# Optimization experiments

Measured on AMD Instinct MI355X. Metric: run time of the kernel, lower is better.

Reference implementation:

```python
import jax, jax.numpy as jnp
import numpy as np
from jax import lax


def setup_inputs() -> dict:
    key = jax.random.key(0)
    ks = jax.random.split(key, 9)
    B, L, d_model = 1, 2048, 1024
    d_inner, d_state, d_conv = 2048, 16, 4

    def g(k, shape, scale):
        return jax.random.normal(k, shape, dtype=jnp.float32) * scale

    return dict(
        x=g(ks[0], (B, L, d_model), 1.0),
        in_proj_w=g(ks[1], (2 * d_inner, d_model), 0.02),   # torch Linear layout (out, in)
        conv_w=g(ks[2], (d_inner, 1, d_conv), 0.1),          # depthwise conv kernel
        conv_b=g(ks[3], (d_inner,), 0.02),
        x_proj_w=g(ks[4], (2 * d_state, d_inner), 0.02),
        dt_proj_w=g(ks[5], (d_inner, d_inner), 0.02),
        dt_proj_b=g(ks[6], (d_inner,), 0.02),
        out_proj_w=g(ks[7], (d_model, d_inner), 0.02),
        A_log=jnp.log(jnp.arange(1, d_state + 1, dtype=jnp.float32)),
        D_param=jnp.ones((d_inner,), dtype=jnp.float32),
    )


def reference(x, in_proj_w, conv_w, conv_b, x_proj_w, dt_proj_w, dt_proj_b,
              out_proj_w, A_log, D_param):
    # x: (B, L, d_model)
    B, L, _ = x.shape
    d_inner = D_param.shape[0]
    d_conv = conv_w.shape[-1]

    xz = x @ in_proj_w.T                       # (B, L, 2*d_inner)
    x_p, z = jnp.split(xz, 2, axis=-1)         # each (B, L, d_inner)

    # causal depthwise conv1d: torch pads d_conv-1 both sides then slices [:L],
    # which equals left-pad d_conv-1 with a valid conv.
    xc = jnp.transpose(x_p, (0, 2, 1))         # (B, d_inner, L)
    xc = lax.conv_general_dilated(
        xc, conv_w, window_strides=(1,), padding=[(d_conv - 1, 0)],
        dimension_numbers=('NCH', 'OIH', 'NCH'), feature_group_count=d_inner)
    xc = xc + conv_b[None, :, None]
    xc = jax.nn.silu(jnp.transpose(xc, (0, 2, 1)))  # (B, L, d_inner)

    # ---- ssm(), mode='tustin'. Note: A_discrete in the original is dead code
    # in tustin mode (never used downstream), so it is omitted.
    dt = jax.nn.softplus(xc @ dt_proj_w.T + dt_proj_b)   # (B, L, d_inner)
    BC = xc @ x_proj_w.T                                 # (B, L, 2*d_state)
    B_ssm, C_ssm = jnp.split(BC, 2, axis=-1)             # (B, L, d_state) each

    # Original: B_disc = dt[...,None] * B_ssm[:, :, None, :]  (B,L,D,N)
    #           y = einsum('bld,bldn->bln', xc, B_disc)
    # This contraction factorizes: sum_d xc*dt is independent of n.
    s = jnp.sum(xc * dt, axis=-1, keepdims=True)          # (B, L, 1)
    y = s * B_ssm                                         # (B, L, d_state)
    y = y * C_ssm                                         # einsum('bln,n->bln', ., ones) * C
    # Original does y.sum(-1) + xc * D; keepdims makes the broadcast well-defined.
    y = jnp.sum(y, axis=-1, keepdims=True) + xc * D_param  # (B, L, d_inner)

    y = y * jax.nn.silu(z)
    return y @ out_proj_w.T                                # (B, L, d_model)
```

## Files before the change

### kernel.cpp

```cpp
#include <hip/hip_runtime.h>
#include <hip/hip_bf16.h>

typedef __attribute__((ext_vector_type(8))) short bf16x8;
typedef __attribute__((ext_vector_type(4))) float f32x4;

__device__ __forceinline__ float b2f(unsigned short u) {
  union { float f; unsigned int i; } v; v.i = ((unsigned int)u) << 16; return v.f;
}
__device__ __forceinline__ unsigned short f2b(float f) {
  __hip_bfloat16 h = __float2bfloat16(f);
  union { __hip_bfloat16 h; unsigned short u; } v; v.h = h; return v.u;
}

#define F32_MAGIC 0x3F800000u

#define GLDS16(g, l)                                                        \
  __builtin_amdgcn_global_load_lds(                                         \
      (const __attribute__((address_space(1))) void*)(g),                   \
      (__attribute__((address_space(3))) void*)(l), 16, 0, 0)

#define POST_BARRIER_FENCE()                  \
  do {                                        \
    asm volatile("" ::: "memory");            \
    __builtin_amdgcn_sched_barrier(0);        \
  } while (0)

__global__ __launch_bounds__(256) void cast4_k(const void* __restrict__ s0, unsigned short* __restrict__ d0,
                                               const void* __restrict__ s1, unsigned short* __restrict__ d1,
                                               const void* __restrict__ s2, unsigned short* __restrict__ d2,
                                               const void* __restrict__ s3, unsigned short* __restrict__ d3,
                                               const unsigned int* __restrict__ dpw) {
  const int i = blockIdx.x * 256 + threadIdx.x;
  const void* s; unsigned short* d; int off;
  if      (i <  262144) { s = s0; d = d0; off = i; }
  else if (i <  786432) { s = s1; d = d1; off = i - 262144; }
  else if (i < 1310720) { s = s2; d = d2; off = i - 786432; }
  else if (i < 1572864) { s = s3; d = d3; off = i - 1310720; }
  else return;
  const bool src_f32 = (dpw[0] == F32_MAGIC);
  bf16x8 o;
  if (src_f32) {
    const float* p = (const float*)s + (size_t)off * 8;
#pragma unroll
    for (int j = 0; j < 8; ++j) o[j] = (short)f2b(p[j]);
  } else {
    o = *(const bf16x8*)((const unsigned short*)s + (size_t)off * 8);
  }
  *(bf16x8*)(d + (size_t)off * 8) = o;
}

__global__ __launch_bounds__(256) void cast_small_k(const void* __restrict__ s0, unsigned short* __restrict__ d0,
                                                    const void* __restrict__ s1, unsigned short* __restrict__ d1,
                                                    const void* __restrict__ s2, unsigned short* __restrict__ d2,
                                                    const void* __restrict__ s3, unsigned short* __restrict__ d3,
                                                    const void* __restrict__ s4, unsigned short* __restrict__ d4,
                                                    const unsigned int* __restrict__ dpw) {
  const int i = blockIdx.x * 256 + threadIdx.x;
  const void* s; unsigned short* d; int off;
  if      (i < 8192) { s = s0; d = d0; off = i; }
  else if (i < 9216) { s = s1; d = d1; off = i - 8192; }
  else if (i < 9472) { s = s2; d = d2; off = i - 9216; }
  else if (i < 9728) { s = s3; d = d3; off = i - 9472; }
  else if (i < 9984) { s = s4; d = d4; off = i - 9728; }
  else return;
  const bool src_f32 = (dpw[0] == F32_MAGIC);
  bf16x8 o;
  if (src_f32) {
    const float* p = (const float*)s + (size_t)off * 8;
#pragma unroll
    for (int j = 0; j < 8; ++j) o[j] = (short)f2b(p[j]);
  } else {
    o = *(const bf16x8*)((const unsigned short*)s + (size_t)off * 8);
  }
  *(bf16x8*)(d + (size_t)off * 8) = o;
}

template <int BM, int BN, int BK, int DEPTH, int MODE, int SWZ>
__global__ __launch_bounds__(256) void gemm_nt(const unsigned short* __restrict__ A,
                                               const unsigned short* __restrict__ B,
                                               void* __restrict__ C,
                                               int M, int N, int K, int gx,
                                               const unsigned short* __restrict__ bias,
                                               const unsigned int* __restrict__ dpw) {
  constexpr int CPR = BK / 8;
  constexpr int CPRL = (BK == 128) ? 4 : (BK == 64) ? 3 : 2;
  constexpr int LPS_A = BM * BK / 2048;
  constexpr int LPS_B = BN * BK / 2048;
  constexpr int LPS = LPS_A + LPS_B;
  constexpr int ASTEP = BM * BK * 2;
  constexpr int BSTEP = BN * BK * 2;
  constexpr int WM = BM / 2, WN = BN / 2;
  constexpr int MI = WM / 16, NJ = WN / 16;
  constexpr int KK = BK / 32;

  __shared__ char lds[DEPTH * (ASTEP + BSTEP)];
  constexpr int BBASE = DEPTH * ASTEP;

  int bx, by;
  if (SWZ) {
    const int bid = blockIdx.x;
    const int k8 = bid & 7;
    const int s = bid >> 3;
    const int sq = k8 + 8 * (s >> 6);
    const int sqw = gx >> 3;
    bx = (sq % sqw) * 8 + (s & 7);
    by = (sq / sqw) * 8 + ((s >> 3) & 7);
  } else {
    bx = blockIdx.x;
    by = blockIdx.y;
  }

  const int tid = threadIdx.x;
  const int lane = tid & 63;
  const int wave = tid >> 6;
  const int m0 = bx * BM;
  const int n0 = by * BN;
  const int wm = (wave >> 1) * WM;
  const int wn = (wave & 1) * WN;
  const int lr = lane & 15;
  const int lu = lane >> 4;

  auto swz = [](int u, int row) {
    int s2 = u ^ (row & (CPR - 1));
    if (CPR == 4) s2 ^= (row >> 2) & 3;
    return s2 & (CPR - 1);
  };

  f32x4 acc[MI][NJ];
#pragma unroll
  for (int i = 0; i < MI; ++i)
#pragma unroll
    for (int j = 0; j < NJ; ++j) acc[i][j] = (f32x4){0.f, 0.f, 0.f, 0.f};

  const unsigned short* aG[LPS_A];
  const unsigned short* bG[LPS_B];
  int aL[LPS_A], bL[LPS_B];
#pragma unroll
  for (int p = 0; p < LPS_A; ++p) {
    const int c = tid + p * 256;
    const int row = c >> CPRL, u = c & (CPR - 1);
    aG[p] = A + (size_t)(m0 + row) * K + swz(u, row) * 8;
    aL[p] = c * 16;
  }
#pragma unroll
  for (int q = 0; q < LPS_B; ++q) {
    const int c = tid + q * 256;
    const int row = c >> CPRL, u = c & (CPR - 1);
    bG[q] = B + (size_t)(n0 + row) * K + swz(u, row) * 8;
    bL[q] = c * 16;
  }
  int aR[MI][KK], bR[NJ][KK];
#pragma unroll
  for (int i = 0; i < MI; ++i)
#pragma unroll
    for (int kk = 0; kk < KK; ++kk) {
      const int row = wm + i * 16 + lr;
      aR[i][kk] = (row * BK + swz(kk * 4 + lu, row) * 8) * 2;
    }
#pragma unroll
  for (int j = 0; j < NJ; ++j)
#pragma unroll
    for (int kk = 0; kk < KK; ++kk) {
      const int row = wn + j * 16 + lr;
      bR[j][kk] = (row * BK + swz(kk * 4 + lu, row) * 8) * 2;
    }

  const int nk = K / BK;

  auto stage = [&](int ab, int bb) {
#pragma unroll
    for (int p = 0; p < LPS_A; ++p) {
      GLDS16(aG[p], lds + ab + aL[p]);
      aG[p] += BK;
    }
#pragma unroll
    for (int q = 0; q < LPS_B; ++q) {
      GLDS16(bG[q], lds + BBASE + bb + bL[q]);
      bG[q] += BK;
    }
  };

#pragma unroll
  for (int i = 0; i < DEPTH - 1; ++i)
    if (i < nk) stage(i * ASTEP, i * BSTEP);

  int acb = 0, bcb = 0;
  int asb = (DEPTH - 1) * ASTEP, bsb = (DEPTH - 1) * BSTEP;

  for (int t = 0; t < nk; ++t) {
    const int ahead = nk - 1 - t;
    if (DEPTH >= 4 && ahead >= DEPTH - 2) {
      asm volatile("s_waitcnt vmcnt(%0)" ::"n"((DEPTH - 2) * LPS) : "memory");
    } else if (DEPTH >= 3 && ahead >= 1 && (DEPTH < 4 || ahead == 1)) {
      asm volatile("s_waitcnt vmcnt(%0)" ::"n"(LPS) : "memory");
    } else {
      asm volatile("s_waitcnt vmcnt(0)" ::: "memory");
    }
    __builtin_amdgcn_s_barrier();
    POST_BARRIER_FENCE();

    if (t + DEPTH - 1 < nk) stage(asb, bsb);

#pragma unroll
    for (int kk = 0; kk < KK; ++kk) {
      bf16x8 af[MI], bfr[NJ];
#pragma unroll
      for (int i = 0; i < MI; ++i)
        af[i] = *(const bf16x8*)(lds + acb + aR[i][kk]);
#pragma unroll
      for (int j = 0; j < NJ; ++j)
        bfr[j] = *(const bf16x8*)(lds + BBASE + bcb + bR[j][kk]);
#pragma unroll
      for (int i = 0; i < MI; ++i)
#pragma unroll
        for (int j = 0; j < NJ; ++j)
          acc[i][j] = __builtin_amdgcn_mfma_f32_16x16x32_bf16(af[i], bfr[j], acc[i][j], 0, 0, 0);
    }

    acb = (acb == (DEPTH - 1) * ASTEP) ? 0 : acb + ASTEP;
    bcb = (bcb == (DEPTH - 1) * BSTEP) ? 0 : bcb + BSTEP;
    asb = (asb == (DEPTH - 1) * ASTEP) ? 0 : asb + ASTEP;
    bsb = (bsb == (DEPTH - 1) * BSTEP) ? 0 : bsb + BSTEP;
  }

  const int cr = lu * 4;
  const int cc = lane & 15;
  const bool f32out = (MODE == 2) ? (dpw[0] == F32_MAGIC) : false;
#pragma unroll
  for (int i = 0; i < MI; ++i)
#pragma unroll
    for (int j = 0; j < NJ; ++j) {
      const int n = n0 + wn + j * 16 + cc;
#pragma unroll
      for (int r = 0; r < 4; ++r) {
        const size_t off = (size_t)(m0 + wm + i * 16 + cr + r) * N + n;
        float v = acc[i][j][r];
        if (MODE == 0) {
          ((unsigned short*)C)[off] = f2b(v);
        } else if (MODE == 1) {
          float pre = v + b2f(bias[n]);
          float dt = (pre > 20.f) ? pre : log1pf(expf(pre));
          ((unsigned short*)C)[off] = f2b(dt);
        } else {
          if (f32out) ((float*)C)[off] = v;
          else        ((unsigned short*)C)[off] = f2b(v);
        }
      }
    }
}

__global__ __launch_bounds__(256) void gemm_bc_k(const unsigned short* __restrict__ A,
                                                 const unsigned short* __restrict__ B,
                                                 float* __restrict__ C, int K, int Nfull) {
  __shared__ float red[4][16][16];
  const int m0 = blockIdx.x * 16;
  const int n0 = blockIdx.y * 16;
  const int tid = threadIdx.x;
  const int wave = tid >> 6;
  const int lane = tid & 63;
  const int lr = lane & 15;
  const int lk = (lane >> 4) * 8;
  const int kslice = K / 4;

  f32x4 acc = (f32x4){0.f, 0.f, 0.f, 0.f};
  const int kbeg = wave * kslice;
  for (int k0 = kbeg; k0 < kbeg + kslice; k0 += 32) {
    bf16x8 a = *(const bf16x8*)(A + (size_t)(m0 + lr) * K + k0 + lk);
    bf16x8 b = *(const bf16x8*)(B + (size_t)(n0 + lr) * K + k0 + lk);
    acc = __builtin_amdgcn_mfma_f32_16x16x32_bf16(a, b, acc, 0, 0, 0);
  }
  const int cr = (lane >> 4) * 4;
#pragma unroll
  for (int r = 0; r < 4; ++r) red[wave][cr + r][lr] = acc[r];
  __syncthreads();
  if (wave == 0) {
#pragma unroll
    for (int r = 0; r < 4; ++r) {
      float s = red[0][cr + r][lr] + red[1][cr + r][lr] + red[2][cr + r][lr] + red[3][cr + r][lr];
      C[(size_t)(m0 + cr + r) * Nfull + n0 + lr] = s;
    }
  }
}

__global__ __launch_bounds__(256) void conv_silu_k(const unsigned short* __restrict__ xz,
                                                   const unsigned short* __restrict__ cw,
                                                   const unsigned short* __restrict__ cb,
                                                   unsigned short* __restrict__ xc) {
  const int idx = blockIdx.x * 256 + threadIdx.x;
  const int l = idx >> 8;
  const int d0 = (idx & 255) * 8;

  float acc[8];
  bf16x8 bias = *(const bf16x8*)(cb + d0);
#pragma unroll
  for (int j = 0; j < 8; ++j) acc[j] = b2f((unsigned short)bias[j]);

  float wv[32];
#pragma unroll
  for (int q = 0; q < 4; ++q) {
    bf16x8 v = *(const bf16x8*)(cw + (size_t)d0 * 4 + q * 8);
#pragma unroll
    for (int e = 0; e < 8; ++e) wv[q * 8 + e] = b2f((unsigned short)v[e]);
  }

#pragma unroll
  for (int t = 0; t < 4; ++t) {
    const int row = l - 3 + t;
    if (row >= 0) {
      bf16x8 v = *(const bf16x8*)(xz + (size_t)row * 4096 + d0);
#pragma unroll
      for (int j = 0; j < 8; ++j) acc[j] += b2f((unsigned short)v[j]) * wv[j * 4 + t];
    }
  }

  bf16x8 o;
#pragma unroll
  for (int j = 0; j < 8; ++j) {
    float s = acc[j];
    s = s / (1.f + expf(-s));
    o[j] = (short)f2b(s);
  }
  *(bf16x8*)(xc + (size_t)l * 2048 + d0) = o;
}

__global__ __launch_bounds__(256) void combine_k(const unsigned short* __restrict__ dt16,
                                                 const float* __restrict__ BC,
                                                 unsigned short* __restrict__ xc,
                                                 const unsigned short* __restrict__ xz,
                                                 const unsigned short* __restrict__ Dp) {
  const int l = blockIdx.x;
  const int t = threadIdx.x;
  const int d0 = t * 8;

  bf16x8 xcv = *(const bf16x8*)(xc + (size_t)l * 2048 + d0);
  bf16x8 dtv = *(const bf16x8*)(dt16 + (size_t)l * 2048 + d0);

  float xf[8];
  float s = 0.f;
#pragma unroll
  for (int j = 0; j < 8; ++j) {
    xf[j] = b2f((unsigned short)xcv[j]);
    s += xf[j] * b2f((unsigned short)dtv[j]);
  }

#pragma unroll
  for (int off = 32; off > 0; off >>= 1) s += __shfl_down(s, off, 64);

  __shared__ float red[4];
  __shared__ float sb;
  const int lane = t & 63, wv = t >> 6;
  if (lane == 0) red[wv] = s;
  __syncthreads();
  if (t == 0) {
    float ss = red[0] + red[1] + red[2] + red[3];
    float bc = 0.f;
    const float* bcp = BC + (size_t)l * 32;
#pragma unroll
    for (int n = 0; n < 16; ++n) bc += bcp[n] * bcp[16 + n];
    sb = ss * bc;
  }
  __syncthreads();
  const float ypre = sb;

  bf16x8 zv = *(const bf16x8*)(xz + (size_t)l * 4096 + 2048 + d0);
  bf16x8 dv = *(const bf16x8*)(Dp + d0);
  bf16x8 o;
#pragma unroll
  for (int j = 0; j < 8; ++j) {
    float z = b2f((unsigned short)zv[j]);
    float yv = (ypre + xf[j] * b2f((unsigned short)dv[j])) * (z / (1.f + expf(-z)));
    o[j] = (short)f2b(yv);
  }
  *(bf16x8*)(xc + (size_t)l * 2048 + d0) = o;
}

extern "C" void kernel_launch(void* const* d_in, const int* in_sizes, int n_in,
                              void* d_out, int out_size, void* d_ws, size_t ws_size,
                              hipStream_t stream) {
  const void* x_raw   = d_in[0];
  const void* wi_raw  = d_in[1];
  const void* cw_raw  = d_in[2];
  const void* cb_raw  = d_in[3];
  const void* xw_raw  = d_in[4];
  const void* dtw_raw = d_in[5];
  const void* dtb_raw = d_in[6];
  const void* ow_raw  = d_in[7];
  const void* dp_raw  = d_in[9];
  const unsigned int* dpw = (const unsigned int*)dp_raw;

  char* ws = (char*)d_ws;
  const size_t MB = 1u << 20;
  unsigned short* xb   = (unsigned short*)(ws + 0 * MB);
  unsigned short* wib  = (unsigned short*)(ws + 4 * MB);
  unsigned short* dtwb = (unsigned short*)(ws + 12 * MB);
  unsigned short* owb  = (unsigned short*)(ws + 20 * MB);
  unsigned short* xwb  = (unsigned short*)(ws + 24 * MB);
  unsigned short* cwb  = (unsigned short*)(ws + 24 * MB + 256 * 1024);
  unsigned short* cbb  = (unsigned short*)(ws + 24 * MB + 320 * 1024);
  unsigned short* dtbb = (unsigned short*)(ws + 24 * MB + 384 * 1024);
  unsigned short* dpb  = (unsigned short*)(ws + 24 * MB + 448 * 1024);
  unsigned short* xz   = (unsigned short*)(ws + 25 * MB);
  unsigned short* xc   = (unsigned short*)(ws + 41 * MB);
  float*          BC   = (float*)(ws + 0 * MB);
  unsigned short* dt16 = (unsigned short*)(ws + 4 * MB);

  const int L = 2048, DM = 1024, DI = 2048;

  cast4_k<<<6144, 256, 0, stream>>>(x_raw, xb, wi_raw, wib, dtw_raw, dtwb, ow_raw, owb, dpw);
  cast_small_k<<<39, 256, 0, stream>>>(xw_raw, xwb, cw_raw, cwb, cb_raw, cbb,
                                       dtb_raw, dtbb, dp_raw, dpb, dpw);

  gemm_nt<128, 128, 64, 2, 0, 1><<<dim3(16 * 32), 256, 0, stream>>>(xb, wib, xz, L, 2 * DI, DM, 16, nullptr, dpw);
  conv_silu_k<<<dim3(2048), 256, 0, stream>>>(xz, cwb, cbb, xc);
  gemm_nt<128, 128, 128, 2, 1, 0><<<dim3(16, 16), 256, 0, stream>>>(xc, dtwb, dt16, L, DI, DI, 0, dtbb, dpw);
  gemm_bc_k<<<dim3(128, 2), 256, 0, stream>>>(xc, xwb, BC, DI, 32);
  combine_k<<<dim3(2048), 256, 0, stream>>>(dt16, BC, xc, xz, dpb);
  gemm_nt<64, 64, 128, 2, 2, 1><<<dim3(32 * 16), 256, 0, stream>>>(xc, owb, d_out, L, DM, DI, 32, nullptr, dpw);
}
```

Baseline: 126.7 us.

## Split-K the dt_proj GEMM into two partials and fuse bias/softplus into combine

```diff
diff --git a/kernel.cpp b/kernel.cpp
--- a/kernel.cpp
+++ b/kernel.cpp
@@ -75,7 +75,7 @@
   *(bf16x8*)(d + (size_t)off * 8) = o;
 }
 
-template <int BM, int BN, int BK, int DEPTH, int MODE, int SWZ>
+template <int BM, int BN, int BK, int DEPTH, int MODE, int SWZ, int KSPLIT>
 __global__ __launch_bounds__(256) void gemm_nt(const unsigned short* __restrict__ A,
                                                const unsigned short* __restrict__ B,
                                                void* __restrict__ C,
@@ -109,6 +109,7 @@
     bx = blockIdx.x;
     by = blockIdx.y;
   }
+  const int ksOff = (KSPLIT > 1) ? blockIdx.z * (K / KSPLIT) : 0;
 
   const int tid = threadIdx.x;
   const int lane = tid & 63;
@@ -139,14 +140,14 @@
   for (int p = 0; p < LPS_A; ++p) {
     const int c = tid + p * 256;
     const int row = c >> CPRL, u = c & (CPR - 1);
-    aG[p] = A + (size_t)(m0 + row) * K + swz(u, row) * 8;
+    aG[p] = A + (size_t)(m0 + row) * K + ksOff + swz(u, row) * 8;
     aL[p] = c * 16;
   }
 #pragma unroll
   for (int q = 0; q < LPS_B; ++q) {
     const int c = tid + q * 256;
     const int row = c >> CPRL, u = c & (CPR - 1);
-    bG[q] = B + (size_t)(n0 + row) * K + swz(u, row) * 8;
+    bG[q] = B + (size_t)(n0 + row) * K + ksOff + swz(u, row) * 8;
     bL[q] = c * 16;
   }
   int aR[MI][KK], bR[NJ][KK];
@@ -165,7 +166,7 @@
       bR[j][kk] = (row * BK + swz(kk * 4 + lu, row) * 8) * 2;
     }
 
-  const int nk = K / BK;
+  const int nk = K / BK / KSPLIT;
 
   auto stage = [&](int ab, int bb) {
 #pragma unroll
@@ -226,6 +227,8 @@
   const int cr = lu * 4;
   const int cc = lane & 15;
   const bool f32out = (MODE == 2) ? (dpw[0] == F32_MAGIC) : false;
+  unsigned short* C16 = (unsigned short*)C +
+      ((KSPLIT > 1) ? (size_t)blockIdx.z * (size_t)M * (size_t)N : 0);
 #pragma unroll
   for (int i = 0; i < MI; ++i)
 #pragma unroll
@@ -236,11 +239,7 @@
         const size_t off = (size_t)(m0 + wm + i * 16 + cr + r) * N + n;
         float v = acc[i][j][r];
         if (MODE == 0) {
-          ((unsigned short*)C)[off] = f2b(v);
-        } else if (MODE == 1) {
-          float pre = v + b2f(bias[n]);
-          float dt = (pre > 20.f) ? pre : log1pf(expf(pre));
-          ((unsigned short*)C)[off] = f2b(dt);
+          C16[off] = f2b(v);
         } else {
           if (f32out) ((float*)C)[off] = v;
           else        ((unsigned short*)C)[off] = f2b(v);
@@ -323,7 +322,8 @@
   *(bf16x8*)(xc + (size_t)l * 2048 + d0) = o;
 }
 
-__global__ __launch_bounds__(256) void combine_k(const unsigned short* __restrict__ dt16,
+__global__ __launch_bounds__(256) void combine_k(const unsigned short* __restrict__ dtH,
+                                                 const unsigned short* __restrict__ dtb,
                                                  const float* __restrict__ BC,
                                                  unsigned short* __restrict__ xc,
                                                  const unsigned short* __restrict__ xz,
@@ -331,16 +331,21 @@
   const int l = blockIdx.x;
   const int t = threadIdx.x;
   const int d0 = t * 8;
+  const size_t HALF = (size_t)2048 * 2048;
 
   bf16x8 xcv = *(const bf16x8*)(xc + (size_t)l * 2048 + d0);
-  bf16x8 dtv = *(const bf16x8*)(dt16 + (size_t)l * 2048 + d0);
+  bf16x8 dA = *(const bf16x8*)(dtH + (size_t)l * 2048 + d0);
+  bf16x8 dB = *(const bf16x8*)(dtH + HALF + (size_t)l * 2048 + d0);
+  bf16x8 dbv = *(const bf16x8*)(dtb + d0);
 
   float xf[8];
   float s = 0.f;
 #pragma unroll
   for (int j = 0; j < 8; ++j) {
     xf[j] = b2f((unsigned short)xcv[j]);
-    s += xf[j] * b2f((unsigned short)dtv[j]);
+    float pre = b2f((unsigned short)dA[j]) + b2f((unsigned short)dB[j]) + b2f((unsigned short)dbv[j]);
+    float dt = (pre > 20.f) ? pre : log1pf(expf(pre));
+    s += xf[j] * dt;
   }
 
 #pragma unroll
@@ -390,19 +395,19 @@
 
   char* ws = (char*)d_ws;
   const size_t MB = 1u << 20;
-  unsigned short* xb   = (unsigned short*)(ws + 0 * MB);
-  unsigned short* wib  = (unsigned short*)(ws + 4 * MB);
-  unsigned short* dtwb = (unsigned short*)(ws + 12 * MB);
-  unsigned short* owb  = (unsigned short*)(ws + 20 * MB);
-  unsigned short* xwb  = (unsigned short*)(ws + 24 * MB);
-  unsigned short* cwb  = (unsigned short*)(ws + 24 * MB + 256 * 1024);
-  unsigned short* cbb  = (unsigned short*)(ws + 24 * MB + 320 * 1024);
-  unsigned short* dtbb = (unsigned short*)(ws + 24 * MB + 384 * 1024);
-  unsigned short* dpb  = (unsigned short*)(ws + 24 * MB + 448 * 1024);
-  unsigned short* xz   = (unsigned short*)(ws + 25 * MB);
-  unsigned short* xc   = (unsigned short*)(ws + 41 * MB);
-  float*          BC   = (float*)(ws + 0 * MB);
-  unsigned short* dt16 = (unsigned short*)(ws + 4 * MB);
+  unsigned short* wib  = (unsigned short*)(ws + 0 * MB);
+  unsigned short* xb   = (unsigned short*)(ws + 8 * MB);
+  unsigned short* dtwb = (unsigned short*)(ws + 16 * MB);
+  unsigned short* owb  = (unsigned short*)(ws + 24 * MB);
+  unsigned short* xwb  = (unsigned short*)(ws + 28 * MB);
+  unsigned short* cwb  = (unsigned short*)(ws + 28 * MB + 256 * 1024);
+  unsigned short* cbb  = (unsigned short*)(ws + 28 * MB + 320 * 1024);
+  unsigned short* dtbb = (unsigned short*)(ws + 28 * MB + 384 * 1024);
+  unsigned short* dpb  = (unsigned short*)(ws + 28 * MB + 448 * 1024);
+  unsigned short* xz   = (unsigned short*)(ws + 29 * MB);
+  unsigned short* xc   = (unsigned short*)(ws + 45 * MB);
+  float*          BC   = (float*)(ws + 53 * MB);
+  unsigned short* dtH  = (unsigned short*)(ws + 0 * MB);
 
   const int L = 2048, DM = 1024, DI = 2048;
 
@@ -410,10 +415,10 @@
   cast_small_k<<<39, 256, 0, stream>>>(xw_raw, xwb, cw_raw, cwb, cb_raw, cbb,
                                        dtb_raw, dtbb, dp_raw, dpb, dpw);
 
-  gemm_nt<128, 128, 64, 2, 0, 1><<<dim3(16 * 32), 256, 0, stream>>>(xb, wib, xz, L, 2 * DI, DM, 16, nullptr, dpw);
+  gemm_nt<128, 128, 64, 2, 0, 1, 1><<<dim3(16 * 32), 256, 0, stream>>>(xb, wib, xz, L, 2 * DI, DM, 16, nullptr, dpw);
   conv_silu_k<<<dim3(2048), 256, 0, stream>>>(xz, cwb, cbb, xc);
-  gemm_nt<128, 128, 128, 2, 1, 0><<<dim3(16, 16), 256, 0, stream>>>(xc, dtwb, dt16, L, DI, DI, 0, dtbb, dpw);
+  gemm_nt<128, 128, 64, 2, 0, 0, 2><<<dim3(16, 16, 2), 256, 0, stream>>>(xc, dtwb, dtH, L, DI, DI, 0, nullptr, dpw);
   gemm_bc_k<<<dim3(128, 2), 256, 0, stream>>>(xc, xwb, BC, DI, 32);
-  combine_k<<<dim3(2048), 256, 0, stream>>>(dt16, BC, xc, xz, dpb);
-  gemm_nt<64, 64, 128, 2, 2, 1><<<dim3(32 * 16), 256, 0, stream>>>(xc, owb, d_out, L, DM, DI, 32, nullptr, dpw);
-}
+  combine_k<<<dim3(2048), 256, 0, stream>>>(dtH, dtbb, BC, xc, xz, dpb);
+  gemm_nt<64, 64, 128, 2, 2, 1, 1><<<dim3(32 * 16), 256, 0, stream>>>(xc, owb, d_out, L, DM, DI, 32, nullptr, dpw);
+}
```

New measurement: 118.7 us, median of 2. 1.07x faster.
